# Kernel optimization log

Measured on AMD Instinct MI355X. Metric: run time of the kernel, lower is better.

## Reference

```python
import jax, jax.numpy as jnp
import numpy as np

B, T, E, H, A, NH = 128, 128, 1024, 1024, 64, 8
SCALE = 1.0 / float(np.sqrt(A))


def setup_inputs() -> dict:
    key = jax.random.key(0)
    ks = jax.random.split(key, 10)
    g = lambda k, shape: jax.random.normal(k, shape, dtype=jnp.float32) * 0.02
    return {
        "encs": jax.random.normal(ks[0], (B, E), dtype=jnp.float32),
        "W_ih": g(ks[1], (3 * H, 2 * E)),
        "W_hh": g(ks[2], (3 * H, H)),
        "b_ih": jnp.zeros((3 * H,), jnp.float32),
        "b_hh": jnp.zeros((3 * H,), jnp.float32),
        "W_mu": g(ks[3], (H, E)),
        "b_mu": jnp.zeros((E,), jnp.float32),
        "W_sig": g(ks[4], (H, E)),
        "b_sig": jnp.zeros((E,), jnp.float32),
        "W_q": g(ks[5], (E, NH * A)),
        "b_q": jnp.zeros((NH * A,), jnp.float32),
        "W_k": g(ks[6], (E, NH * A)),
        "b_k": jnp.zeros((NH * A,), jnp.float32),
        "W_v": g(ks[7], (E, NH * A)),
        "b_v": jnp.zeros((NH * A,), jnp.float32),
        "W_o": g(ks[8], (NH * A, E)),
        "b_o": jnp.zeros((E,), jnp.float32),
    }


def reference(encs, W_ih, W_hh, b_ih, b_hh, W_mu, b_mu, W_sig, b_sig,
              W_q, b_q, W_k, b_k, W_v, b_v, W_o, b_o):
    noise_key = jax.random.key(1234)

    def gru(x, h):  # torch.nn.GRUCell math
        gi = x @ W_ih.T + b_ih
        gh = h @ W_hh.T + b_hh
        ir, iz, inn = jnp.split(gi, 3, axis=-1)
        hr, hz, hn = jnp.split(gh, 3, axis=-1)
        r = jax.nn.sigmoid(ir + hr)
        z = jax.nn.sigmoid(iz + hz)
        n = jnp.tanh(inn + r * hn)
        return (1.0 - z) * n + z * h

    def attn_last(s, i):
        # multi_attn(s,s,s)[:, i]: only row i of softmax is needed (rows independent)
        q = (s[:, :, :] @ W_q + b_q)  # (B,T,NH*A)
        q_i = jax.lax.dynamic_index_in_dim(q, i, axis=1, keepdims=False).reshape(B, NH, A)
        k = (s @ W_k + b_k).reshape(B, T, NH, A)
        v = (s @ W_v + b_v).reshape(B, T, NH, A)
        scores = jnp.einsum("bha,bjha->bhj", q_i, k) * SCALE  # (B,NH,T)
        valid = jnp.arange(T) <= i
        scores = jnp.where(valid[None, None, :], scores, -1e30)
        w = jax.nn.softmax(scores, axis=-1)
        ctx = jnp.einsum("bhj,bjha->bha", w, v).reshape(B, NH * A)
        return ctx @ W_o + b_o  # (B,E)

    def step(carry, i):
        h, mus, sigs, context = carry
        x = jnp.concatenate([encs, context], axis=-1)  # (B,2E)
        h = gru(x, h)
        mu = h @ W_mu + b_mu
        sig = jax.nn.softplus(h @ W_sig + b_sig)
        mus = mus.at[:, i].set(mu)
        sigs = sigs.at[:, i].set(sig)
        eps = jax.random.normal(jax.random.fold_in(noise_key, i), (B, T, E), dtype=jnp.float32)
        valid = (jnp.arange(T) <= i)[None, :, None]
        s = jnp.where(valid, mus + eps * sigs, 0.0)
        context = attn_last(s, i)
        return (h, mus, sigs, context), None

    init = (jnp.zeros((B, H), jnp.float32),
            jnp.zeros((B, T, E), jnp.float32),
            jnp.zeros((B, T, E), jnp.float32),
            jnp.zeros((B, E), jnp.float32))
    (h, mus, sigs, _), _ = jax.lax.scan(step, init, jnp.arange(T))
    # final return is s sampled at step T-1 (all positions valid)
    eps_last = jax.random.normal(jax.random.fold_in(noise_key, T - 1), (B, T, E), dtype=jnp.float32)
    return mus + eps_last * sigs
```

## Files before the change

### kernel.cpp

```cpp
#include <hip/hip_runtime.h>

#define B_   128
#define T_   128
#define E_   1024
#define H_   1024
#define A_   64
#define NH_  8
#define G_   3072
#define QK_  512
#define SCALE_ 0.125f

__device__ __forceinline__ unsigned rotl32(unsigned x, int r) {
  return (x << r) | (x >> (32 - r));
}

__device__ __forceinline__ void tf2x32(unsigned k0, unsigned k1,
                                       unsigned x0, unsigned x1,
                                       unsigned& o0, unsigned& o1) {
  unsigned k2 = k0 ^ k1 ^ 0x1BD11BDAu;
  x0 += k0; x1 += k1;
  x0 += x1; x1 = rotl32(x1, 13); x1 ^= x0;
  x0 += x1; x1 = rotl32(x1, 15); x1 ^= x0;
  x0 += x1; x1 = rotl32(x1, 26); x1 ^= x0;
  x0 += x1; x1 = rotl32(x1,  6); x1 ^= x0;
  x0 += k1; x1 += k2 + 1u;
  x0 += x1; x1 = rotl32(x1, 17); x1 ^= x0;
  x0 += x1; x1 = rotl32(x1, 29); x1 ^= x0;
  x0 += x1; x1 = rotl32(x1, 16); x1 ^= x0;
  x0 += x1; x1 = rotl32(x1, 24); x1 ^= x0;
  x0 += k2; x1 += k0 + 2u;
  x0 += x1; x1 = rotl32(x1, 13); x1 ^= x0;
  x0 += x1; x1 = rotl32(x1, 15); x1 ^= x0;
  x0 += x1; x1 = rotl32(x1, 26); x1 ^= x0;
  x0 += x1; x1 = rotl32(x1,  6); x1 ^= x0;
  x0 += k0; x1 += k1 + 3u;
  x0 += x1; x1 = rotl32(x1, 17); x1 ^= x0;
  x0 += x1; x1 = rotl32(x1, 29); x1 ^= x0;
  x0 += x1; x1 = rotl32(x1, 16); x1 ^= x0;
  x0 += x1; x1 = rotl32(x1, 24); x1 ^= x0;
  x0 += k1; x1 += k2 + 4u;
  x0 += x1; x1 = rotl32(x1, 13); x1 ^= x0;
  x0 += x1; x1 = rotl32(x1, 15); x1 ^= x0;
  x0 += x1; x1 = rotl32(x1, 26); x1 ^= x0;
  x0 += x1; x1 = rotl32(x1,  6); x1 ^= x0;
  x0 += k2; x1 += k0 + 5u;
  o0 = x0; o1 = x1;
}

__device__ __forceinline__ float bits_to_normal(unsigned bits) {
  float uf = __uint_as_float((bits >> 9) | 0x3F800000u) - 1.0f;
  const float LO = -0.99999994f;
  float u = fmaxf(LO, uf * 2.0f + LO);
  float w = -log1pf(-u * u);
  float p;
  if (w < 5.0f) {
    w -= 2.5f;
    p = 2.81022636e-08f;
    p = fmaf(p, w, 3.43273939e-07f);
    p = fmaf(p, w, -3.5233877e-06f);
    p = fmaf(p, w, -4.39150654e-06f);
    p = fmaf(p, w, 0.00021858087f);
    p = fmaf(p, w, -0.00125372503f);
    p = fmaf(p, w, -0.00417768164f);
    p = fmaf(p, w, 0.246640727f);
    p = fmaf(p, w, 1.50140941f);
  } else {
    w = sqrtf(w) - 3.0f;
    p = -0.000200214257f;
    p = fmaf(p, w, 0.000100950558f);
    p = fmaf(p, w, 0.00134934322f);
    p = fmaf(p, w, -0.00367342844f);
    p = fmaf(p, w, 0.00573950773f);
    p = fmaf(p, w, -0.0076224613f);
    p = fmaf(p, w, 0.00943887047f);
    p = fmaf(p, w, 1.00167406f);
    p = fmaf(p, w, 2.83297682f);
  }
  return 1.41421356f * p * u;
}

__device__ __forceinline__ float sigmoidf_(float x) {
  return 1.0f / (1.0f + expf(-x));
}

__device__ __forceinline__ float ld_elem(const void* p, long i, int isb) {
  if (isb) {
    unsigned short u = ((const unsigned short*)p)[i];
    return __uint_as_float(((unsigned)u) << 16);
  }
  return ((const float*)p)[i];
}

__global__ __launch_bounds__(256) void sniff_kernel(const void* encs, int* flag) {
  __shared__ int cnt;
  if (threadIdx.x == 0) cnt = 0;
  __syncthreads();
  const unsigned* w = (const unsigned*)encs;
  int c = 0;
  for (int i = threadIdx.x; i < 4096; i += 256) {
    unsigned e7 = (w[i] >> 8) & 0x7F;
    if (e7 >= 0x3B && e7 <= 0x41) c++;
  }
  atomicAdd(&cnt, c);
  __syncthreads();
  if (threadIdx.x == 0) flag[0] = (cnt > 2048) ? 1 : 0;
}

__global__ __launch_bounds__(256) void conv_kernel(const void* src, float* dst,
                                                   long n, const int* flag) {
  long i = (long)blockIdx.x * 256 + threadIdx.x;
  int isb = flag[0];
  if (i < n) dst[i] = ld_elem(src, i, isb);
}

__global__ __launch_bounds__(256) void trans_kernel(
    const void* W_ih, const void* W_hh, const void* W_mu, const void* W_sig,
    const void* W_k, const float* __restrict__ bihF, const float* __restrict__ bhhF,
    float* __restrict__ Wbig, float* __restrict__ Wms, float* __restrict__ WkT,
    float* __restrict__ Wenc4, float* __restrict__ bias4,
    float* __restrict__ xh, float* __restrict__ h, unsigned* __restrict__ skeys,
    const int* flag)
{
  long idx = (long)blockIdx.x * 256 + threadIdx.x;
  int y = blockIdx.y;
  int isb = flag[0];
  if (y == 0) {
    if (idx < 4194304) {
      int e = (int)(idx & 1023); int col = (int)(idx >> 10);
      int j = col >> 2, c = col & 3;
      float v = 0.f;
      if (c < 3) v = ld_elem(W_ih, (long)(c * 1024 + j) * 2048 + 1024 + e, isb);
      Wbig[(long)e * 4096 + col] = v;
    }
  } else if (y == 1) {
    if (idx < 4194304) {
      int e = (int)(idx & 1023); int col = (int)(idx >> 10);
      int j = col >> 2, c = col & 3;
      float v = 0.f;
      if (c == 0)      v = ld_elem(W_hh, (long)j * 1024 + e, isb);
      else if (c == 1) v = ld_elem(W_hh, (long)(1024 + j) * 1024 + e, isb);
      else if (c == 3) v = ld_elem(W_hh, (long)(2048 + j) * 1024 + e, isb);
      Wbig[(long)(1024 + e) * 4096 + col] = v;
    }
  } else if (y == 2) {
    if (idx < 2097152) {
      int k = (int)(idx >> 11), n = (int)(idx & 2047);
      float v = (n < 1024) ? ld_elem(W_mu, (long)k * 1024 + n, isb)
                           : ld_elem(W_sig, (long)k * 1024 + (n - 1024), isb);
      Wms[idx] = v;
    }
  } else if (y == 3) {
    if (idx < 524288) {
      int qk = (int)(idx >> 10), e = (int)(idx & 1023);
      WkT[idx] = ld_elem(W_k, (long)e * 512 + qk, isb);
    }
    if (idx < 4096) {
      int j = (int)(idx >> 2), c = (int)(idx & 3);
      float v;
      if (c == 0)      v = bihF[j] + bhhF[j];
      else if (c == 1) v = bihF[1024 + j] + bhhF[1024 + j];
      else if (c == 2) v = bihF[2048 + j];
      else             v = bhhF[2048 + j];
      bias4[idx] = v;
    }
    if (idx < 262144) xh[idx] = 0.f;
    if (idx < 131072) h[idx] = 0.f;
    if (idx < 128) {
      unsigned o0, o1;
      tf2x32(0u, 1234u, 0u, (unsigned)idx, o0, o1);
      skeys[2 * idx] = o0; skeys[2 * idx + 1] = o1;
    }
  } else {
    if (idx < 4194304) {
      int e = (int)(idx & 1023); int col = (int)(idx >> 10);
      int j = col >> 2, c = col & 3;
      float v = 0.f;
      if (c < 3) v = ld_elem(W_ih, (long)(c * 1024 + j) * 2048 + e, isb);
      Wenc4[(long)e * 4096 + col] = v;
    }
  }
}

__global__ __launch_bounds__(256) void consts_kernel(
    const float* __restrict__ bqF, const float* __restrict__ bkF,
    const float* __restrict__ bvF, const float* __restrict__ boF,
    const float* __restrict__ WkT, const float* __restrict__ WoF,
    float* __restrict__ bqk, float* __restrict__ qbc, float* __restrict__ bvo)
{
  int idx = blockIdx.x * 256 + threadIdx.x;
  int hh = idx >> 10, e = idx & 1023;
  float s = 0.f;
  for (int a = 0; a < 64; ++a)
    s += bqF[hh * 64 + a] * WkT[(long)(hh * 64 + a) * 1024 + e];
  bqk[idx] = s;
  if (idx < 1024) {
    float v = boF[idx];
    for (int ha = 0; ha < 512; ++ha) v += bvF[ha] * WoF[(long)ha * 1024 + idx];
    bvo[idx] = v;
  }
  if (idx < 8) {
    float v = 0.f;
    for (int a = 0; a < 64; ++a) v += bqF[idx * 64 + a] * bkF[idx * 64 + a];
    qbc[idx] = v;
  }
}

__device__ void mm128_dev(float* smem,
    const float* A, long lda, long zA, int nsumA, long psA,
    const float* Bm, long ldb, long zB,
    float* C, long ldc, long zC, long pstride,
    int Ktot, int S, int bx, int by, int zz, int tid)
{
  int head = zz / S, sp = zz - head * S;
  int Kc = Ktot / S;
  long kb = (long)sp * Kc;
  A += (long)head * zA;
  Bm += (long)head * zB;
  C += (long)head * zC + (long)sp * pstride;
  long m0 = (long)by * 128;
  long n0 = (long)bx * 128;
  float* As = smem;
  float* Bs = smem + 2112;
  int tx = tid & 15, ty = tid >> 4;
  int am = tid >> 2, ac = tid & 3;
  int bk = tid >> 5, bn = tid & 31;
  float acc[8][8];
  #pragma unroll
  for (int i = 0; i < 8; ++i)
    #pragma unroll
    for (int j = 0; j < 8; ++j) acc[i][j] = 0.f;

  for (int k0 = 0; k0 < Kc; k0 += 16) {
    const float* Ap0 = A + (m0 + am) * lda + kb + k0 + 4 * ac;
    const float* Ap1 = A + (m0 + am + 64) * lda + kb + k0 + 4 * ac;
    float4 a0 = *(const float4*)Ap0;
    float4 a1 = *(const float4*)Ap1;
    for (int s2 = 1; s2 < nsumA; ++s2) {
      float4 t0 = *(const float4*)(Ap0 + (long)s2 * psA);
      float4 t1 = *(const float4*)(Ap1 + (long)s2 * psA);
      a0.x += t0.x; a0.y += t0.y; a0.z += t0.z; a0.w += t0.w;
      a1.x += t1.x; a1.y += t1.y; a1.z += t1.z; a1.w += t1.w;
    }
    float4 b0 = *(const float4*)(Bm + (kb + k0 + bk) * ldb + n0 + 4 * bn);
    float4 b1 = *(const float4*)(Bm + (kb + k0 + bk + 8) * ldb + n0 + 4 * bn);
    __syncthreads();
    As[(4 * ac + 0) * 132 + am] = a0.x; As[(4 * ac + 1) * 132 + am] = a0.y;
    As[(4 * ac + 2) * 132 + am] = a0.z; As[(4 * ac + 3) * 132 + am] = a0.w;
    As[(4 * ac + 0) * 132 + am + 64] = a1.x; As[(4 * ac + 1) * 132 + am + 64] = a1.y;
    As[(4 * ac + 2) * 132 + am + 64] = a1.z; As[(4 * ac + 3) * 132 + am + 64] = a1.w;
    *(float4*)&Bs[bk * 132 + 4 * bn] = b0;
    *(float4*)&Bs[(bk + 8) * 132 + 4 * bn] = b1;
    __syncthreads();
    #pragma unroll
    for (int kk = 0; kk < 16; ++kk) {
      float4 av0 = *(const float4*)&As[kk * 132 + ty * 4];
      float4 av1 = *(const float4*)&As[kk * 132 + 64 + ty * 4];
      float4 bv0 = *(const float4*)&Bs[kk * 132 + tx * 4];
      float4 bv1 = *(const float4*)&Bs[kk * 132 + 64 + tx * 4];
      float amv[8] = {av0.x, av0.y, av0.z, av0.w, av1.x, av1.y, av1.z, av1.w};
      float bnv[8] = {bv0.x, bv0.y, bv0.z, bv0.w, bv1.x, bv1.y, bv1.z, bv1.w};
      #pragma unroll
      for (int i = 0; i < 8; ++i)
        #pragma unroll
        for (int j = 0; j < 8; ++j)
          acc[i][j] = fmaf(amv[i], bnv[j], acc[i][j]);
    }
  }

  #pragma unroll
  for (int i = 0; i < 8; ++i) {
    long r = m0 + (long)(i >> 2) * 64 + ty * 4 + (i & 3);
    float4 v0 = {acc[i][0], acc[i][1], acc[i][2], acc[i][3]};
    float4 v1 = {acc[i][4], acc[i][5], acc[i][6], acc[i][7]};
    *(float4*)(C + r * ldc + n0 + tx * 4) = v0;
    *(float4*)(C + r * ldc + n0 + 64 + tx * 4) = v1;
  }
}

__global__ __launch_bounds__(256) void mm128(
    const float* A, long lda, long zA, int nsumA, long psA,
    const float* Bm, long ldb, long zB,
    float* C, long ldc, long zC, long pstride, int Ktot, int S)
{
  __shared__ __align__(16) float smem[4224];
  mm128_dev(smem, A, lda, zA, nsumA, psA, Bm, ldb, zB, C, ldc, zC, pstride,
            Ktot, S, blockIdx.x, blockIdx.y, blockIdx.z, threadIdx.x);
}

__global__ __launch_bounds__(256) void mm64s(
    const float* __restrict__ A, long lda, long zA,
    const float* __restrict__ Bm, long ldb, long zB,
    float* __restrict__ C, long ldc, long zC, long pstride,
    int Ktot, int S)
{
  int zz = blockIdx.z;
  int head = zz / S, sp = zz - head * S;
  int Kc = Ktot / S;
  long kb = (long)sp * Kc;
  A += (long)head * zA; Bm += (long)head * zB;
  C += (long)head * zC + (long)sp * pstride;
  long n0 = (long)blockIdx.x * 64;
  long m0 = (long)blockIdx.y * 64;
  __shared__ float As[16][68];
  __shared__ float Bs[16][68];
  int tid = threadIdx.x;
  int tx = tid & 15, ty = tid >> 4;
  int ar = tid >> 2, ac = tid & 3;
  int br = tid >> 4, bc = tid & 15;
  float acc[4][4];
  #pragma unroll
  for (int i = 0; i < 4; ++i)
    #pragma unroll
    for (int j = 0; j < 4; ++j) acc[i][j] = 0.f;

  for (int k0 = 0; k0 < Kc; k0 += 16) {
    float4 a4 = *(const float4*)(A + (m0 + ar) * lda + kb + k0 + 4 * ac);
    float4 b4 = *(const float4*)(Bm + (kb + k0 + br) * ldb + n0 + 4 * bc);
    __syncthreads();
    As[4 * ac + 0][ar] = a4.x; As[4 * ac + 1][ar] = a4.y;
    As[4 * ac + 2][ar] = a4.z; As[4 * ac + 3][ar] = a4.w;
    *(float4*)(&Bs[br][4 * bc]) = b4;
    __syncthreads();
    #pragma unroll
    for (int kk = 0; kk < 16; ++kk) {
      float4 av = *(const float4*)(&As[kk][4 * ty]);
      float4 bv = *(const float4*)(&Bs[kk][4 * tx]);
      float amv[4] = {av.x, av.y, av.z, av.w};
      float bnv[4] = {bv.x, bv.y, bv.z, bv.w};
      #pragma unroll
      for (int im = 0; im < 4; ++im)
        #pragma unroll
        for (int jn = 0; jn < 4; ++jn)
          acc[im][jn] = fmaf(amv[im], bnv[jn], acc[im][jn]);
    }
  }
  #pragma unroll
  for (int im = 0; im < 4; ++im) {
    long m = m0 + ty * 4 + im;
    float4 v = {acc[im][0], acc[im][1], acc[im][2], acc[im][3]};
    *(float4*)(C + m * ldc + n0 + tx * 4) = v;
  }
}

__device__ void gen_rows(int lo, int hi, int lbid, int nb, int step,
                         const float* __restrict__ mus,
                         const float* __restrict__ sigs,
                         float* __restrict__ s,
                         const unsigned* __restrict__ skeys, int tid) {
  int nvb = (hi - lo) * 128;
  if (nvb <= 0) return;
  unsigned sk0 = skeys[2 * step], sk1 = skeys[2 * step + 1];
  for (int vb = lbid; vb < nvb; vb += nb) {
    int t = lo + (vb >> 7);
    int b = vb & 127;
    int e = tid * 4;
    unsigned f = (unsigned)(b * (T_ * E_) + t * E_ + e);
    unsigned o0, o1;
    float nv[4];
    tf2x32(sk0, sk1, 0u, f + 0u, o0, o1); nv[0] = bits_to_normal(o0 ^ o1);
    tf2x32(sk0, sk1, 0u, f + 1u, o0, o1); nv[1] = bits_to_normal(o0 ^ o1);
    tf2x32(sk0, sk1, 0u, f + 2u, o0, o1); nv[2] = bits_to_normal(o0 ^ o1);
    tf2x32(sk0, sk1, 0u, f + 3u, o0, o1); nv[3] = bits_to_normal(o0 ^ o1);
    long i4 = (((long)b * T_ + t) * E_ + e) >> 2;
    float4 mu = ((const float4*)mus)[i4];
    float4 sg = ((const float4*)sigs)[i4];
    float4 out;
    out.x = fmaf(nv[0], sg.x, mu.x);
    out.y = fmaf(nv[1], sg.y, mu.y);
    out.z = fmaf(nv[2], sg.z, mu.z);
    out.w = fmaf(nv[3], sg.w, mu.w);
    ((float4*)s)[i4] = out;
  }
}

__global__ __launch_bounds__(256) void g1gen_kernel(
    const float* __restrict__ xh, const float* __restrict__ Wbig,
    float* __restrict__ gsumP,
    const float* __restrict__ mus, const float* __restrict__ sigs,
    float* __restrict__ s, const unsigned* __restrict__ skeys, int step)
{
  __shared__ __align__(16) float smem[4224];
  int bid = blockIdx.x, tid = threadIdx.x;
  if (bid < 256) {
    mm128_dev(smem, xh, 2048, 0, 1, 0, Wbig, 4096, 0,
              gsumP, 4096, 0, 524288, 2048, 8, bid & 31, 0, bid >> 5, tid);
  } else {
    int r1 = (2 * step) / 3;
    gen_rows(0, r1, bid - 256, 256, step, mus, sigs, s, skeys, tid);
  }
}

__global__ __launch_bounds__(256) void gru_epi(
    const float* __restrict__ gsumP, const float* __restrict__ gie4,
    const float* __restrict__ bias4, float* __restrict__ h,
    float* __restrict__ xh)
{
  int idx = blockIdx.x * 256 + threadIdx.x;
  int b = idx >> 10, j = idx & 1023;
  float4 v = ((const float4*)gie4)[(long)b * 1024 + j];
  float4 bb = ((const float4*)bias4)[j];
  v.x += bb.x; v.y += bb.y; v.z += bb.z; v.w += bb.w;
  #pragma unroll
  for (int s = 0; s < 8; ++s) {
    float4 t = ((const float4*)gsumP)[(long)s * 131072 + (long)b * 1024 + j];
    v.x += t.x; v.y += t.y; v.z += t.z; v.w += t.w;
  }
  float r = sigmoidf_(v.x);
  float z = sigmoidf_(v.y);
  float n = tanhf(v.z + r * v.w);
  float ho = h[idx];
  float hn = (1.0f - z) * n + z * ho;
  h[idx] = hn;
  xh[(long)b * 2048 + 1024 + j] = hn;
}

__global__ __launch_bounds__(256) void g2gen_kernel(
    const float* __restrict__ hbuf, const float* __restrict__ Wms,
    float* __restrict__ musigP,
    const float* __restrict__ mus, const float* __restrict__ sigs,
    float* __restrict__ s, const unsigned* __restrict__ skeys, int step)
{
  __shared__ __align__(16) float smem[4224];
  int bid = blockIdx.x, tid = threadIdx.x;
  if (bid < 128) {
    mm128_dev(smem, hbuf, 1024, 0, 1, 0, Wms, 2048, 0,
              musigP, 2048, 0, 262144, 1024, 8, bid & 15, 0, bid >> 4, tid);
  } else {
    int r1 = (2 * step) / 3;
    gen_rows(r1, step, bid - 128, 128, step, mus, sigs, s, skeys, tid);
  }
}

__global__ __launch_bounds__(256) void msgen_kernel(
    const float* __restrict__ musigP, const float* __restrict__ bmuF,
    const float* __restrict__ bsigF, float* __restrict__ mus,
    float* __restrict__ sigs, float* __restrict__ s,
    const unsigned* __restrict__ skeys, int step)
{
  int el = blockIdx.x * 256 + threadIdx.x;
  int b = el >> 10, e = el & 1023;
  float mu = bmuF[e], xg = bsigF[e];
  #pragma unroll
  for (int s2 = 0; s2 < 8; ++s2) {
    mu += musigP[(long)s2 * 262144 + (long)b * 2048 + e];
    xg += musigP[(long)s2 * 262144 + (long)b * 2048 + 1024 + e];
  }
  float sig = fmaxf(xg, 0.0f) + log1pf(expf(-fabsf(xg)));
  long o = ((long)b * T_ + step) * E_ + e;
  mus[o] = mu;
  sigs[o] = sig;
  unsigned sk0 = skeys[2 * step], sk1 = skeys[2 * step + 1];
  unsigned f = (unsigned)(b * (T_ * E_) + step * E_ + e);
  unsigned o0, o1;
  tf2x32(sk0, sk1, 0u, f, o0, o1);
  s[o] = fmaf(bits_to_normal(o0 ^ o1), sig, mu);
}

__global__ __launch_bounds__(256) void t_kernel(
    const float* __restrict__ qP, const float* __restrict__ WkT,
    const float* __restrict__ bkF, const float* __restrict__ bqk,
    const float* __restrict__ qbc, float* __restrict__ tmat,
    float* __restrict__ qb)
{
  int e = blockIdx.x * 256 + threadIdx.x;
  int hh = blockIdx.y;
  int b0 = blockIdx.z * 8;
  __shared__ float q_l[8][64];
  int tid = threadIdx.x;
  for (int idx2 = tid; idx2 < 512; idx2 += 256) {
    int bb = idx2 >> 6, a = idx2 & 63;
    float v = 0.f;
    #pragma unroll
    for (int s = 0; s < 8; ++s)
      v += qP[(long)s * 65536 + (long)(b0 + bb) * 512 + hh * 64 + a];
    q_l[bb][a] = v;
  }
  __syncthreads();
  float acc[8];
  #pragma unroll
  for (int bb = 0; bb < 8; ++bb) acc[bb] = 0.f;
  for (int a = 0; a < 64; ++a) {
    float wv = WkT[(long)(hh * 64 + a) * 1024 + e];
    #pragma unroll
    for (int bb = 0; bb < 8; ++bb) acc[bb] = fmaf(q_l[bb][a], wv, acc[bb]);
  }
  float bq_ = bqk[hh * 1024 + e];
  #pragma unroll
  for (int bb = 0; bb < 8; ++bb)
    tmat[((long)(b0 + bb) * NH_ + hh) * 1024 + e] = acc[bb] + bq_;
  if (blockIdx.x == 0 && tid < 8) {
    int bb = tid;
    float sm = qbc[hh];
    for (int a = 0; a < 64; ++a) sm += q_l[bb][a] * bkF[hh * 64 + a];
    qb[(b0 + bb) * NH_ + hh] = sm;
  }
}

__global__ __launch_bounds__(256) void scores_kernel(
    const float* __restrict__ s, const float* __restrict__ tmat,
    const float* __restrict__ qb, float* __restrict__ scg, int step)
{
  int b = blockIdx.y;
  int jbase = blockIdx.x * 32;
  __shared__ float s_ch[32][132];
  __shared__ float t_ch[8][132];
  int tid = threadIdx.x;
  int hh = tid >> 5, jj = tid & 31;
  int j = jbase + jj;
  float acc = 0.f;
  for (int e0 = 0; e0 < 1024; e0 += 128) {
    __syncthreads();
    #pragma unroll
    for (int q = 0; q < 4; ++q) {
      int f = tid + q * 256;
      int jr = f >> 5, e4 = f & 31;
      int jg = jbase + jr;
      if (jg <= step)
        *(float4*)&s_ch[jr][e4 * 4] =
            *(const float4*)&s[((long)b * T_ + jg) * E_ + e0 + e4 * 4];
    }
    {
      int e4 = tid & 31, h2 = tid >> 5;
      *(float4*)&t_ch[h2][e4 * 4] =
          *(const float4*)&tmat[((long)b * NH_ + h2) * E_ + e0 + e4 * 4];
    }
    __syncthreads();
    if (j <= step) {
      #pragma unroll
      for (int e4 = 0; e4 < 32; ++e4) {
        float4 sv = *(const float4*)&s_ch[jj][e4 * 4];
        float4 tv = *(const float4*)&t_ch[hh][e4 * 4];
        acc = fmaf(sv.x, tv.x, acc);
        acc = fmaf(sv.y, tv.y, acc);
        acc = fmaf(sv.z, tv.z, acc);
        acc = fmaf(sv.w, tv.w, acc);
      }
    }
  }
  if (j <= step)
    scg[((long)b * NH_ + hh) * T_ + j] = (acc + qb[b * NH_ + hh]) * SCALE_;
}

__global__ __launch_bounds__(256) void ctx_kernel(
    const float* __restrict__ s, const float* __restrict__ scg,
    float* __restrict__ ctxE, int step)
{
  int b = blockIdx.y;
  int et = blockIdx.x;
  __shared__ float w_l[NH_][T_];
  __shared__ float s_l[32][68];
  int tid = threadIdx.x;
  {
    int hh = tid >> 5, l = tid & 31;
    const float* sc = scg + ((long)b * NH_ + hh) * T_;
    float m = -3.0e38f;
    for (int j = l; j <= step; j += 32) m = fmaxf(m, sc[j]);
    for (int off = 16; off; off >>= 1) m = fmaxf(m, __shfl_xor(m, off, 32));
    float d = 0.f;
    for (int j = l; j <= step; j += 32) {
      float pe = expf(sc[j] - m);
      w_l[hh][j] = pe;
      d += pe;
    }
    for (int off = 16; off; off >>= 1) d += __shfl_xor(d, off, 32);
    float inv = 1.0f / d;
    for (int j = l; j <= step; j += 32) w_l[hh][j] *= inv;
  }
  int e = tid & 63, hp = tid >> 6;
  float acc0 = 0.f, acc1 = 0.f;
  for (int jc = 0; jc <= step; jc += 32) {
    __syncthreads();
    #pragma unroll
    for (int q = 0; q < 8; ++q) {
      int f = tid + q * 256;
      int jr = f >> 6, ee = f & 63;
      int jg = jc + jr;
      if (jg <= step)
        s_l[jr][ee] = s[((long)b * T_ + jg) * E_ + et * 64 + ee];
    }
    __syncthreads();
    int jmax = min(31, step - jc);
    for (int jr = 0; jr <= jmax; ++jr) {
      float sv = s_l[jr][e];
      acc0 = fmaf(w_l[hp][jc + jr], sv, acc0);
      acc1 = fmaf(w_l[hp + 4][jc + jr], sv, acc1);
    }
  }
  ctxE[((long)b * NH_ + hp) * E_ + et * 64 + e] = acc0;
  ctxE[((long)b * NH_ + hp + 4) * E_ + et * 64 + e] = acc1;
}

__global__ __launch_bounds__(256) void o_kernel(
    const float* __restrict__ ctxhP, const float* __restrict__ Wo,
    const float* __restrict__ bvo, float* __restrict__ xh)
{
  long n0 = (long)blockIdx.x * 64;
  long m0 = (long)blockIdx.y * 64;
  __shared__ float As[16][68];
  __shared__ float Bs[16][68];
  int tid = threadIdx.x;
  int tx = tid & 15, ty = tid >> 4;
  int ar = tid >> 2, ac = tid & 3;
  int br = tid >> 4, bc = tid & 15;
  float acc[4][4];
  #pragma unroll
  for (int i = 0; i < 4; ++i)
    #pragma unroll
    for (int j = 0; j < 4; ++j) acc[i][j] = 0.f;

  for (int k0 = 0; k0 < 512; k0 += 16) {
    const float* Ap = ctxhP + (m0 + ar) * 512 + k0 + 4 * ac;
    float4 a4 = *(const float4*)Ap;
    #pragma unroll
    for (int s2 = 1; s2 < 4; ++s2) {
      float4 t = *(const float4*)(Ap + (long)s2 * 65536);
      a4.x += t.x; a4.y += t.y; a4.z += t.z; a4.w += t.w;
    }
    float4 b4 = *(const float4*)(Wo + (k0 + br) * 1024 + n0 + 4 * bc);
    __syncthreads();
    As[4 * ac + 0][ar] = a4.x; As[4 * ac + 1][ar] = a4.y;
    As[4 * ac + 2][ar] = a4.z; As[4 * ac + 3][ar] = a4.w;
    *(float4*)(&Bs[br][4 * bc]) = b4;
    __syncthreads();
    #pragma unroll
    for (int kk = 0; kk < 16; ++kk) {
      float4 av = *(const float4*)(&As[kk][4 * ty]);
      float4 bv = *(const float4*)(&Bs[kk][4 * tx]);
      float amv[4] = {av.x, av.y, av.z, av.w};
      float bnv[4] = {bv.x, bv.y, bv.z, bv.w};
      #pragma unroll
      for (int im = 0; im < 4; ++im)
        #pragma unroll
        for (int jn = 0; jn < 4; ++jn)
          acc[im][jn] = fmaf(amv[im], bnv[jn], acc[im][jn]);
    }
  }
  float4 bq = ((const float4*)bvo)[(n0 + tx * 4) >> 2];
  #pragma unroll
  for (int im = 0; im < 4; ++im) {
    long m = m0 + ty * 4 + im;
    float4 v = {acc[im][0] + bq.x, acc[im][1] + bq.y,
                acc[im][2] + bq.z, acc[im][3] + bq.w};
    *(float4*)(xh + m * 2048 + n0 + tx * 4) = v;
  }
}

extern "C" void kernel_launch(void* const* d_in, const int* in_sizes, int n_in,
                              void* d_out, int out_size, void* d_ws, size_t ws_size,
                              hipStream_t stream) {
  (void)in_sizes; (void)n_in; (void)out_size; (void)ws_size;
  const void* encs  = d_in[0];
  const void* W_ih  = d_in[1];
  const void* W_hh  = d_in[2];
  const void* b_ih  = d_in[3];
  const void* b_hh  = d_in[4];
  const void* W_mu  = d_in[5];
  const void* b_mu  = d_in[6];
  const void* W_sig = d_in[7];
  const void* b_sig = d_in[8];
  const void* W_q   = d_in[9];
  const void* b_q   = d_in[10];
  const void* W_k   = d_in[11];
  const void* b_k   = d_in[12];
  const void* W_v   = d_in[13];
  const void* b_v   = d_in[14];
  const void* W_o   = d_in[15];
  const void* b_o   = d_in[16];

  float* s = (float*)d_out;
  float* w = (float*)d_ws;

  int*   flag   = (int*)w;
  float* p      = w + 1024;
  float* WbigF  = p;  p += (size_t)2048 * 4096;
  float* WmsF   = p;  p += (size_t)1024 * 2048;
  float* WkTF   = p;  p += (size_t)512 * 1024;
  float* WqF    = p;  p += (size_t)1024 * 512;
  float* WvF    = p;  p += (size_t)1024 * 512;
  float* WoF    = p;  p += (size_t)512 * 1024;
  float* encsF  = p;  p += (size_t)B_ * E_;
  float* bihF   = p;  p += 4096;
  float* bhhF   = p;  p += 4096;
  float* bmuF   = p;  p += 1024;
  float* bsigF  = p;  p += 1024;
  float* bqF    = p;  p += 1024;
  float* bkF    = p;  p += 1024;
  float* bvF    = p;  p += 1024;
  float* boF    = p;  p += 1024;
  float* bias4  = p;  p += 4096;
  float* bqk    = p;  p += 8192;
  float* qbc    = p;  p += 1024;
  float* bvo    = p;  p += 1024;
  unsigned* skeys = (unsigned*)p; p += 1024;
  float* gie4   = p;  p += (size_t)B_ * 4096;
  float* xh     = p;  p += (size_t)B_ * 2048;
  float* hbuf   = p;  p += (size_t)B_ * 1024;
  float* gsumP  = p;  p += (size_t)8 * B_ * 4096;
  float* musigP = p;  p += (size_t)8 * B_ * 2048;
  float* qP     = p;  p += (size_t)8 * B_ * 512;
  float* tmat   = p;  p += (size_t)B_ * NH_ * E_;
  float* qbv    = p;  p += 1024;
  float* scg    = p;  p += (size_t)B_ * NH_ * T_;
  float* ctxE   = p;  p += (size_t)B_ * NH_ * E_;
  float* ctxhP  = p;  p += (size_t)4 * B_ * 512;
  float* mus    = p;  p += (size_t)B_ * T_ * E_;
  float* sigs   = p;  p += (size_t)B_ * T_ * E_;
  float* Wenc4  = gsumP;

  sniff_kernel<<<1, 256, 0, stream>>>(encs, flag);
  auto conv = [&](const void* src, float* dst, long n) {
    conv_kernel<<<dim3((unsigned)((n + 255) / 256)), 256, 0, stream>>>(src, dst, n, flag);
  };
  conv(encs,  encsF, (long)B_ * E_);
  conv(b_ih,  bihF,  G_);
  conv(b_hh,  bhhF,  G_);
  conv(b_mu,  bmuF,  1024);
  conv(b_sig, bsigF, 1024);
  conv(b_q,   bqF,   512);
  conv(b_k,   bkF,   512);
  conv(b_v,   bvF,   512);
  conv(b_o,   boF,   1024);
  conv(W_q,   WqF,   (long)1024 * 512);
  conv(W_v,   WvF,   (long)1024 * 512);
  conv(W_o,   WoF,   (long)512 * 1024);

  trans_kernel<<<dim3(16384, 5), 256, 0, stream>>>(
      W_ih, W_hh, W_mu, W_sig, W_k, bihF, bhhF,
      WbigF, WmsF, WkTF, Wenc4, bias4, xh, hbuf, skeys, flag);
  consts_kernel<<<dim3(32), 256, 0, stream>>>(
      bqF, bkF, bvF, boF, WkTF, WoF, bqk, qbc, bvo);
  mm128<<<dim3(32, 1, 1), 256, 0, stream>>>(
      encsF, 1024, 0, 1, 0, Wenc4, 4096, 0, gie4, 4096, 0, 0, 1024, 1);

  for (int i = 0; i < T_; ++i) {
    g1gen_kernel<<<dim3(512), 256, 0, stream>>>(
        xh, WbigF, gsumP, mus, sigs, s, skeys, i);
    gru_epi<<<dim3(512), 256, 0, stream>>>(gsumP, gie4, bias4, hbuf, xh);
    g2gen_kernel<<<dim3(256), 256, 0, stream>>>(
        hbuf, WmsF, musigP, mus, sigs, s, skeys, i);
    msgen_kernel<<<dim3(512), 256, 0, stream>>>(
        musigP, bmuF, bsigF, mus, sigs, s, skeys, i);
    mm64s<<<dim3(8, 2, 8), 256, 0, stream>>>(
        s + (long)i * E_, (long)T_ * E_, 0, WqF, 512, 0,
        qP, 512, 0, 65536, 1024, 8);
    t_kernel<<<dim3(4, 8, 16), 256, 0, stream>>>(
        qP, WkTF, bkF, bqk, qbc, tmat, qbv);
    scores_kernel<<<dim3((i + 32) / 32, B_), 256, 0, stream>>>(
        s, tmat, qbv, scg, i);
    ctx_kernel<<<dim3(16, B_), 256, 0, stream>>>(s, scg, ctxE, i);
    mm64s<<<dim3(1, 2, 32), 256, 0, stream>>>(
        ctxE, 8192, 1024, WvF, 512, 64, ctxhP, 512, 64, 65536, 1024, 4);
    o_kernel<<<dim3(16, 2), 256, 0, stream>>>(ctxhP, WoF, bvo, xh);
  }
}
```

Measured before the change: 33.83 ms.

## Unfuse noise generation from GEMMs and fuse scores with context into one attention kernel

The old g1gen/g2gen kernels, which ran the GRU and mu/sigma GEMMs alongside row-split noise sampling, are replaced. Noise sampling now runs as its own gen_s kernel before the GEMMs, and the GEMMs become plain mm128 launches. The separate scores and context kernels are merged into one attn_kernel per batch row, split into two halves over E. It keeps the score vector in shared memory, which removes the scg global round trip and one launch. The trade-off is far fewer blocks for attention (2×128 instead of 16×128), and each half recomputes the scores, so parallelism drops and score work is duplicated.

After: 35.53 ms. 1.05x slower.

```diff
diff --git a/kernel.cpp b/kernel.cpp
--- a/kernel.cpp
+++ b/kernel.cpp
@@ -205,22 +205,24 @@
   }
 }
 
-__device__ void mm128_dev(float* smem,
-    const float* A, long lda, long zA, int nsumA, long psA,
-    const float* Bm, long ldb, long zB,
-    float* C, long ldc, long zC, long pstride,
-    int Ktot, int S, int bx, int by, int zz, int tid)
-{
+__global__ __launch_bounds__(256) void mm128(
+    const float* __restrict__ A, long lda, long zA, int nsumA, long psA,
+    const float* __restrict__ Bm, long ldb, long zB,
+    float* __restrict__ C, long ldc, long zC, long pstride,
+    int Ktot, int S)
+{
+  int zz = blockIdx.z;
   int head = zz / S, sp = zz - head * S;
   int Kc = Ktot / S;
   long kb = (long)sp * Kc;
   A += (long)head * zA;
   Bm += (long)head * zB;
   C += (long)head * zC + (long)sp * pstride;
-  long m0 = (long)by * 128;
-  long n0 = (long)bx * 128;
-  float* As = smem;
-  float* Bs = smem + 2112;
+  long m0 = (long)blockIdx.y * 128;
+  long n0 = (long)blockIdx.x * 128;
+  __shared__ float As[16][132];
+  __shared__ float Bs[16][132];
+  int tid = threadIdx.x;
   int tx = tid & 15, ty = tid >> 4;
   int am = tid >> 2, ac = tid & 3;
   int bk = tid >> 5, bn = tid & 31;
@@ -244,19 +246,19 @@
     float4 b0 = *(const float4*)(Bm + (kb + k0 + bk) * ldb + n0 + 4 * bn);
     float4 b1 = *(const float4*)(Bm + (kb + k0 + bk + 8) * ldb + n0 + 4 * bn);
     __syncthreads();
-    As[(4 * ac + 0) * 132 + am] = a0.x; As[(4 * ac + 1) * 132 + am] = a0.y;
-    As[(4 * ac + 2) * 132 + am] = a0.z; As[(4 * ac + 3) * 132 + am] = a0.w;
-    As[(4 * ac + 0) * 132 + am + 64] = a1.x; As[(4 * ac + 1) * 132 + am + 64] = a1.y;
-    As[(4 * ac + 2) * 132 + am + 64] = a1.z; As[(4 * ac + 3) * 132 + am + 64] = a1.w;
-    *(float4*)&Bs[bk * 132 + 4 * bn] = b0;
-    *(float4*)&Bs[(bk + 8) * 132 + 4 * bn] = b1;
+    As[4 * ac + 0][am] = a0.x; As[4 * ac + 1][am] = a0.y;
+    As[4 * ac + 2][am] = a0.z; As[4 * ac + 3][am] = a0.w;
+    As[4 * ac + 0][am + 64] = a1.x; As[4 * ac + 1][am + 64] = a1.y;
+    As[4 * ac + 2][am + 64] = a1.z; As[4 * ac + 3][am + 64] = a1.w;
+    *(float4*)&Bs[bk][4 * bn] = b0;
+    *(float4*)&Bs[bk + 8][4 * bn] = b1;
     __syncthreads();
     #pragma unroll
     for (int kk = 0; kk < 16; ++kk) {
-      float4 av0 = *(const float4*)&As[kk * 132 + ty * 4];
-      float4 av1 = *(const float4*)&As[kk * 132 + 64 + ty * 4];
-      float4 bv0 = *(const float4*)&Bs[kk * 132 + tx * 4];
-      float4 bv1 = *(const float4*)&Bs[kk * 132 + 64 + tx * 4];
+      float4 av0 = *(const float4*)&As[kk][ty * 4];
+      float4 av1 = *(const float4*)&As[kk][64 + ty * 4];
+      float4 bv0 = *(const float4*)&Bs[kk][tx * 4];
+      float4 bv1 = *(const float4*)&Bs[kk][64 + tx * 4];
       float amv[8] = {av0.x, av0.y, av0.z, av0.w, av1.x, av1.y, av1.z, av1.w};
       float bnv[8] = {bv0.x, bv0.y, bv0.z, bv0.w, bv1.x, bv1.y, bv1.z, bv1.w};
       #pragma unroll
@@ -275,16 +277,6 @@
     *(float4*)(C + r * ldc + n0 + tx * 4) = v0;
     *(float4*)(C + r * ldc + n0 + 64 + tx * 4) = v1;
   }
-}
-
-__global__ __launch_bounds__(256) void mm128(
-    const float* A, long lda, long zA, int nsumA, long psA,
-    const float* Bm, long ldb, long zB,
-    float* C, long ldc, long zC, long pstride, int Ktot, int S)
-{
-  __shared__ __align__(16) float smem[4224];
-  mm128_dev(smem, A, lda, zA, nsumA, psA, Bm, ldb, zB, C, ldc, zC, pstride,
-            Ktot, S, blockIdx.x, blockIdx.y, blockIdx.z, threadIdx.x);
 }
 
 __global__ __launch_bounds__(256) void mm64s(
@@ -342,54 +334,6 @@
   }
 }
 
-__device__ void gen_rows(int lo, int hi, int lbid, int nb, int step,
-                         const float* __restrict__ mus,
-                         const float* __restrict__ sigs,
-                         float* __restrict__ s,
-                         const unsigned* __restrict__ skeys, int tid) {
-  int nvb = (hi - lo) * 128;
-  if (nvb <= 0) return;
-  unsigned sk0 = skeys[2 * step], sk1 = skeys[2 * step + 1];
-  for (int vb = lbid; vb < nvb; vb += nb) {
-    int t = lo + (vb >> 7);
-    int b = vb & 127;
-    int e = tid * 4;
-    unsigned f = (unsigned)(b * (T_ * E_) + t * E_ + e);
-    unsigned o0, o1;
-    float nv[4];
-    tf2x32(sk0, sk1, 0u, f + 0u, o0, o1); nv[0] = bits_to_normal(o0 ^ o1);
-    tf2x32(sk0, sk1, 0u, f + 1u, o0, o1); nv[1] = bits_to_normal(o0 ^ o1);
-    tf2x32(sk0, sk1, 0u, f + 2u, o0, o1); nv[2] = bits_to_normal(o0 ^ o1);
-    tf2x32(sk0, sk1, 0u, f + 3u, o0, o1); nv[3] = bits_to_normal(o0 ^ o1);
-    long i4 = (((long)b * T_ + t) * E_ + e) >> 2;
-    float4 mu = ((const float4*)mus)[i4];
-    float4 sg = ((const float4*)sigs)[i4];
-    float4 out;
-    out.x = fmaf(nv[0], sg.x, mu.x);
-    out.y = fmaf(nv[1], sg.y, mu.y);
-    out.z = fmaf(nv[2], sg.z, mu.z);
-    out.w = fmaf(nv[3], sg.w, mu.w);
-    ((float4*)s)[i4] = out;
-  }
-}
-
-__global__ __launch_bounds__(256) void g1gen_kernel(
-    const float* __restrict__ xh, const float* __restrict__ Wbig,
-    float* __restrict__ gsumP,
-    const float* __restrict__ mus, const float* __restrict__ sigs,
-    float* __restrict__ s, const unsigned* __restrict__ skeys, int step)
-{
-  __shared__ __align__(16) float smem[4224];
-  int bid = blockIdx.x, tid = threadIdx.x;
-  if (bid < 256) {
-    mm128_dev(smem, xh, 2048, 0, 1, 0, Wbig, 4096, 0,
-              gsumP, 4096, 0, 524288, 2048, 8, bid & 31, 0, bid >> 5, tid);
-  } else {
-    int r1 = (2 * step) / 3;
-    gen_rows(0, r1, bid - 256, 256, step, mus, sigs, s, skeys, tid);
-  }
-}
-
 __global__ __launch_bounds__(256) void gru_epi(
     const float* __restrict__ gsumP, const float* __restrict__ gie4,
     const float* __restrict__ bias4, float* __restrict__ h,
@@ -412,23 +356,6 @@
   float hn = (1.0f - z) * n + z * ho;
   h[idx] = hn;
   xh[(long)b * 2048 + 1024 + j] = hn;
-}
-
-__global__ __launch_bounds__(256) void g2gen_kernel(
-    const float* __restrict__ hbuf, const float* __restrict__ Wms,
-    float* __restrict__ musigP,
-    const float* __restrict__ mus, const float* __restrict__ sigs,
-    float* __restrict__ s, const unsigned* __restrict__ skeys, int step)
-{
-  __shared__ __align__(16) float smem[4224];
-  int bid = blockIdx.x, tid = threadIdx.x;
-  if (bid < 128) {
-    mm128_dev(smem, hbuf, 1024, 0, 1, 0, Wms, 2048, 0,
-              musigP, 2048, 0, 262144, 1024, 8, bid & 15, 0, bid >> 4, tid);
-  } else {
-    int r1 = (2 * step) / 3;
-    gen_rows(r1, step, bid - 128, 128, step, mus, sigs, s, skeys, tid);
-  }
 }
 
 __global__ __launch_bounds__(256) void msgen_kernel(
@@ -456,6 +383,32 @@
   s[o] = fmaf(bits_to_normal(o0 ^ o1), sig, mu);
 }
 
+__global__ __launch_bounds__(256) void gen_s(
+    const float* __restrict__ mus, const float* __restrict__ sigs,
+    float* __restrict__ s, const unsigned* __restrict__ skeys, int step)
+{
+  int t = blockIdx.x;
+  int b = blockIdx.y;
+  int e = threadIdx.x * 4;
+  unsigned sk0 = skeys[2 * step], sk1 = skeys[2 * step + 1];
+  unsigned f = (unsigned)(b * (T_ * E_) + t * E_ + e);
+  unsigned o0, o1;
+  float nv[4];
+  tf2x32(sk0, sk1, 0u, f + 0u, o0, o1); nv[0] = bits_to_normal(o0 ^ o1);
+  tf2x32(sk0, sk1, 0u, f + 1u, o0, o1); nv[1] = bits_to_normal(o0 ^ o1);
+  tf2x32(sk0, sk1, 0u, f + 2u, o0, o1); nv[2] = bits_to_normal(o0 ^ o1);
+  tf2x32(sk0, sk1, 0u, f + 3u, o0, o1); nv[3] = bits_to_normal(o0 ^ o1);
+  long i4 = (((long)b * T_ + t) * E_ + e) >> 2;
+  float4 mu = ((const float4*)mus)[i4];
+  float4 sg = ((const float4*)sigs)[i4];
+  float4 out;
+  out.x = fmaf(nv[0], sg.x, mu.x);
+  out.y = fmaf(nv[1], sg.y, mu.y);
+  out.z = fmaf(nv[2], sg.z, mu.z);
+  out.w = fmaf(nv[3], sg.w, mu.w);
+  ((float4*)s)[i4] = out;
+}
+
 __global__ __launch_bounds__(256) void t_kernel(
     const float* __restrict__ qP, const float* __restrict__ WkT,
     const float* __restrict__ bkF, const float* __restrict__ bqk,
@@ -496,98 +449,93 @@
   }
 }
 
-__global__ __launch_bounds__(256) void scores_kernel(
+__global__ __launch_bounds__(256) void attn_kernel(
     const float* __restrict__ s, const float* __restrict__ tmat,
-    const float* __restrict__ qb, float* __restrict__ scg, int step)
+    const float* __restrict__ qb, float* __restrict__ ctxE, int step)
 {
   int b = blockIdx.y;
-  int jbase = blockIdx.x * 32;
+  int half = blockIdx.x;
+  __shared__ float t_l[NH_][1024];
   __shared__ float s_ch[32][132];
-  __shared__ float t_ch[8][132];
-  int tid = threadIdx.x;
-  int hh = tid >> 5, jj = tid & 31;
-  int j = jbase + jj;
-  float acc = 0.f;
-  for (int e0 = 0; e0 < 1024; e0 += 128) {
-    __syncthreads();
-    #pragma unroll
-    for (int q = 0; q < 4; ++q) {
-      int f = tid + q * 256;
-      int jr = f >> 5, e4 = f & 31;
-      int jg = jbase + jr;
-      if (jg <= step)
-        *(float4*)&s_ch[jr][e4 * 4] =
-            *(const float4*)&s[((long)b * T_ + jg) * E_ + e0 + e4 * 4];
-    }
-    {
-      int e4 = tid & 31, h2 = tid >> 5;
-      *(float4*)&t_ch[h2][e4 * 4] =
-          *(const float4*)&tmat[((long)b * NH_ + h2) * E_ + e0 + e4 * 4];
-    }
-    __syncthreads();
-    if (j <= step) {
-      #pragma unroll
-      for (int e4 = 0; e4 < 32; ++e4) {
-        float4 sv = *(const float4*)&s_ch[jj][e4 * 4];
-        float4 tv = *(const float4*)&t_ch[hh][e4 * 4];
-        acc = fmaf(sv.x, tv.x, acc);
-        acc = fmaf(sv.y, tv.y, acc);
-        acc = fmaf(sv.z, tv.z, acc);
-        acc = fmaf(sv.w, tv.w, acc);
-      }
-    }
-  }
-  if (j <= step)
-    scg[((long)b * NH_ + hh) * T_ + j] = (acc + qb[b * NH_ + hh]) * SCALE_;
-}
-
-__global__ __launch_bounds__(256) void ctx_kernel(
-    const float* __restrict__ s, const float* __restrict__ scg,
-    float* __restrict__ ctxE, int step)
-{
-  int b = blockIdx.y;
-  int et = blockIdx.x;
   __shared__ float w_l[NH_][T_];
   __shared__ float s_l[32][68];
   int tid = threadIdx.x;
+  for (int k = tid; k < 2048; k += 256)
+    ((float4*)&t_l[0][0])[k] = ((const float4*)&tmat[(long)b * NH_ * E_])[k];
+  __syncthreads();
+  int hh = tid >> 5, jj = tid & 31;
+  float qbv_ = qb[b * NH_ + hh];
+  int njt = (step + 32) / 32;
+  for (int jt = 0; jt < njt; ++jt) {
+    int jbase = jt * 32;
+    int j = jbase + jj;
+    float acc = 0.f;
+    for (int e0 = 0; e0 < 1024; e0 += 128) {
+      __syncthreads();
+      #pragma unroll
+      for (int q = 0; q < 4; ++q) {
+        int f = tid + q * 256;
+        int jr = f >> 5, e4 = f & 31;
+        int jg = jbase + jr;
+        if (jg <= step)
+          *(float4*)&s_ch[jr][e4 * 4] =
+              *(const float4*)&s[((long)b * T_ + jg) * E_ + e0 + e4 * 4];
+      }
+      __syncthreads();
+      if (j <= step) {
+        #pragma unroll
+        for (int e4 = 0; e4 < 32; ++e4) {
+          float4 sv = *(const float4*)&s_ch[jj][e4 * 4];
+          float4 tv = *(const float4*)&t_l[hh][e0 + e4 * 4];
+          acc = fmaf(sv.x, tv.x, acc);
+          acc = fmaf(sv.y, tv.y, acc);
+          acc = fmaf(sv.z, tv.z, acc);
+          acc = fmaf(sv.w, tv.w, acc);
+        }
+      }
+    }
+    if (j <= step) w_l[hh][j] = (acc + qbv_) * SCALE_;
+  }
+  __syncthreads();
   {
-    int hh = tid >> 5, l = tid & 31;
-    const float* sc = scg + ((long)b * NH_ + hh) * T_;
+    int l = jj;
     float m = -3.0e38f;
-    for (int j = l; j <= step; j += 32) m = fmaxf(m, sc[j]);
+    for (int j2 = l; j2 <= step; j2 += 32) m = fmaxf(m, w_l[hh][j2]);
     for (int off = 16; off; off >>= 1) m = fmaxf(m, __shfl_xor(m, off, 32));
     float d = 0.f;
-    for (int j = l; j <= step; j += 32) {
-      float pe = expf(sc[j] - m);
-      w_l[hh][j] = pe;
+    for (int j2 = l; j2 <= step; j2 += 32) {
+      float pe = expf(w_l[hh][j2] - m);
+      w_l[hh][j2] = pe;
       d += pe;
     }
     for (int off = 16; off; off >>= 1) d += __shfl_xor(d, off, 32);
     float inv = 1.0f / d;
-    for (int j = l; j <= step; j += 32) w_l[hh][j] *= inv;
+    for (int j2 = l; j2 <= step; j2 += 32) w_l[hh][j2] *= inv;
   }
   int e = tid & 63, hp = tid >> 6;
-  float acc0 = 0.f, acc1 = 0.f;
-  for (int jc = 0; jc <= step; jc += 32) {
-    __syncthreads();
-    #pragma unroll
-    for (int q = 0; q < 8; ++q) {
-      int f = tid + q * 256;
-      int jr = f >> 6, ee = f & 63;
-      int jg = jc + jr;
-      if (jg <= step)
-        s_l[jr][ee] = s[((long)b * T_ + jg) * E_ + et * 64 + ee];
-    }
-    __syncthreads();
-    int jmax = min(31, step - jc);
-    for (int jr = 0; jr <= jmax; ++jr) {
-      float sv = s_l[jr][e];
-      acc0 = fmaf(w_l[hp][jc + jr], sv, acc0);
-      acc1 = fmaf(w_l[hp + 4][jc + jr], sv, acc1);
-    }
-  }
-  ctxE[((long)b * NH_ + hp) * E_ + et * 64 + e] = acc0;
-  ctxE[((long)b * NH_ + hp + 4) * E_ + et * 64 + e] = acc1;
+  for (int et = half * 8; et < half * 8 + 8; ++et) {
+    float acc0 = 0.f, acc1 = 0.f;
+    for (int jc = 0; jc <= step; jc += 32) {
+      __syncthreads();
+      #pragma unroll
+      for (int q = 0; q < 8; ++q) {
+        int f = tid + q * 256;
+        int jr = f >> 6, ee = f & 63;
+        int jg = jc + jr;
+        if (jg <= step)
+          s_l[jr][ee] = s[((long)b * T_ + jg) * E_ + et * 64 + ee];
+      }
+      __syncthreads();
+      int jmax = min(31, step - jc);
+      for (int jr = 0; jr <= jmax; ++jr) {
+        float sv = s_l[jr][e];
+        acc0 = fmaf(w_l[hp][jc + jr], sv, acc0);
+        acc1 = fmaf(w_l[hp + 4][jc + jr], sv, acc1);
+      }
+    }
+    ctxE[((long)b * NH_ + hp) * E_ + et * 64 + e] = acc0;
+    ctxE[((long)b * NH_ + hp + 4) * E_ + et * 64 + e] = acc1;
+  }
 }
 
 __global__ __launch_bounds__(256) void o_kernel(
@@ -700,7 +648,6 @@
   float* qP     = p;  p += (size_t)8 * B_ * 512;
   float* tmat   = p;  p += (size_t)B_ * NH_ * E_;
   float* qbv    = p;  p += 1024;
-  float* scg    = p;  p += (size_t)B_ * NH_ * T_;
   float* ctxE   = p;  p += (size_t)B_ * NH_ * E_;
   float* ctxhP  = p;  p += (size_t)4 * B_ * 512;
   float* mus    = p;  p += (size_t)B_ * T_ * E_;
@@ -733,11 +680,13 @@
       encsF, 1024, 0, 1, 0, Wenc4, 4096, 0, gie4, 4096, 0, 0, 1024, 1);
 
   for (int i = 0; i < T_; ++i) {
-    g1gen_kernel<<<dim3(512), 256, 0, stream>>>(
-        xh, WbigF, gsumP, mus, sigs, s, skeys, i);
+    if (i > 0)
+      gen_s<<<dim3(i, B_), 256, 0, stream>>>(mus, sigs, s, skeys, i);
+    mm128<<<dim3(32, 1, 8), 256, 0, stream>>>(
+        xh, 2048, 0, 1, 0, WbigF, 4096, 0, gsumP, 4096, 0, 524288, 2048, 8);
     gru_epi<<<dim3(512), 256, 0, stream>>>(gsumP, gie4, bias4, hbuf, xh);
-    g2gen_kernel<<<dim3(256), 256, 0, stream>>>(
-        hbuf, WmsF, musigP, mus, sigs, s, skeys, i);
+    mm128<<<dim3(16, 1, 8), 256, 0, stream>>>(
+        hbuf, 1024, 0, 1, 0, WmsF, 2048, 0, musigP, 2048, 0, 262144, 1024, 8);
     msgen_kernel<<<dim3(512), 256, 0, stream>>>(
         musigP, bmuF, bsigF, mus, sigs, s, skeys, i);
     mm64s<<<dim3(8, 2, 8), 256, 0, stream>>>(
@@ -745,9 +694,7 @@
         qP, 512, 0, 65536, 1024, 8);
     t_kernel<<<dim3(4, 8, 16), 256, 0, stream>>>(
         qP, WkTF, bkF, bqk, qbc, tmat, qbv);
-    scores_kernel<<<dim3((i + 32) / 32, B_), 256, 0, stream>>>(
-        s, tmat, qbv, scg, i);
-    ctx_kernel<<<dim3(16, B_), 256, 0, stream>>>(s, scg, ctxE, i);
+    attn_kernel<<<dim3(2, B_), 256, 0, stream>>>(s, tmat, qbv, ctxE, i);
     mm64s<<<dim3(1, 2, 32), 256, 0, stream>>>(
         ctxE, 8192, 1024, WvF, 512, 64, ctxhP, 512, 64, 65536, 1024, 4);
     o_kernel<<<dim3(16, 2), 256, 0, stream>>>(ctxhP, WoF, bvo, xh);
```
